# Optimization experiments

Measured on AMD Instinct MI355X. Metric: run time of the kernel, lower is better.

Reference implementation:

```python
import jax, jax.numpy as jnp
import numpy as np

DIM = 512
NUM_CLASSES = 2048
BATCH = 16384


def setup_inputs() -> dict:
    key = jax.random.key(0)
    kx, kc = jax.random.split(key)
    x = jax.random.normal(kx, (BATCH, DIM), dtype=jnp.float32)
    # torch.rand -> uniform [0,1)
    centers = jax.random.uniform(kc, (NUM_CLASSES, DIM), dtype=jnp.float32)
    return {"x": x, "centers": centers}


def reference(x, centers):
    x_sq = jnp.sum(x * x, axis=-1, keepdims=True)            # [B, 1]
    c_sq = jnp.sum(centers * centers, axis=-1)[None, :]      # [1, K]
    cross = jnp.einsum('bd,kd->bk', x, centers)              # [B, K]
    dist_sq = x_sq + c_sq - 2.0 * cross                      # [B, K]
    # responsibilities: stable softmax over -0.5 * dist_sq along classes
    resp = jax.nn.softmax(-0.5 * dist_sq, axis=-1)
    return resp
```

## Files before the change

### kernel.cpp

```cpp
#include <hip/hip_runtime.h>

#define BATCH 16384
#define DIM   512
#define NCLS  2048

typedef _Float16 half8 __attribute__((ext_vector_type(8)));
typedef float    floatx4 __attribute__((ext_vector_type(4)));

__global__ __launch_bounds__(256) void pack_b(const float* __restrict__ C,
                                              _Float16* __restrict__ BP) {
    int t = blockIdx.x * 256 + threadIdx.x;
    int lane = t & 63, ns = t >> 6;
    int s = ns & 15, n = ns >> 4;
    int col = n * 16 + (lane & 15);
    int k   = s * 32 + (lane >> 4) * 8;
    const float4* src = reinterpret_cast<const float4*>(C + (size_t)col * DIM + k);
    float4 a = src[0], b = src[1];
    half8 h;
    h[0] = (_Float16)a.x; h[1] = (_Float16)a.y; h[2] = (_Float16)a.z; h[3] = (_Float16)a.w;
    h[4] = (_Float16)b.x; h[5] = (_Float16)b.y; h[6] = (_Float16)b.z; h[7] = (_Float16)b.w;
    *reinterpret_cast<half8*>(BP + (size_t)t * 8) = h;
}

__global__ __launch_bounds__(64) void csq_kernel(const float* __restrict__ c,
                                                 float* __restrict__ hcsq) {
    int k = blockIdx.x, t = threadIdx.x;
    const float4* p = reinterpret_cast<const float4*>(c + (size_t)k * DIM);
    float s = 0.f;
    #pragma unroll
    for (int j = 0; j < 2; ++j) {
        float4 v = p[t + j * 64];
        s += v.x * v.x + v.y * v.y + v.z * v.z + v.w * v.w;
    }
    #pragma unroll
    for (int o = 32; o; o >>= 1) s += __shfl_xor(s, o);
    if (t == 0) hcsq[k] = 0.5f * s;
}

__global__ __launch_bounds__(512, 2) void fused_kernel(
    const float* __restrict__ X,
    const _Float16* __restrict__ BP,
    const float* __restrict__ hcsq,
    float* __restrict__ O)
{
    __shared__ __align__(16) _Float16 As[32 * 512];
    __shared__ float redm[8][32];
    __shared__ float rsum[8][32];

    const int tid  = threadIdx.x;
    const int lane = tid & 63;
    const int wave = tid >> 6;
    const int l4   = lane >> 4;
    const int r15  = lane & 15;

    for (int tile = 0; tile < 2; ++tile) {
        const int rowB = (blockIdx.x * 2 + tile) * 32;

        #pragma unroll
        for (int i = 0; i < 4; ++i) {
            int G = i * 512 + tid;
            int row = G >> 6, g = G & 63;
            const float* src = X + (size_t)(rowB + row) * DIM + g * 8;
            float4 a = *reinterpret_cast<const float4*>(src);
            float4 b = *reinterpret_cast<const float4*>(src + 4);
            half8 h;
            h[0] = (_Float16)a.x; h[1] = (_Float16)a.y; h[2] = (_Float16)a.z; h[3] = (_Float16)a.w;
            h[4] = (_Float16)b.x; h[5] = (_Float16)b.y; h[6] = (_Float16)b.z; h[7] = (_Float16)b.w;
            *reinterpret_cast<half8*>(&As[(row * 64 + (g ^ (row & 7))) * 8]) = h;
        }
        __syncthreads();

        floatx4 logv[4][2][4];
        float mj[2][4];
        #pragma unroll
        for (int rt = 0; rt < 2; ++rt)
            #pragma unroll
            for (int j = 0; j < 4; ++j) mj[rt][j] = -1e30f;

        #pragma unroll
        for (int chunk = 0; chunk < 4; ++chunk) {
            floatx4 acc[2][4];
            #pragma unroll
            for (int rt = 0; rt < 2; ++rt)
                #pragma unroll
                for (int ct = 0; ct < 4; ++ct)
                    acc[rt][ct] = (floatx4){0.f, 0.f, 0.f, 0.f};

            float hc[4];
            #pragma unroll
            for (int ct = 0; ct < 4; ++ct)
                hc[ct] = hcsq[chunk * 512 + wave * 64 + ct * 16 + r15];

            const _Float16* bb = BP + ((size_t)(chunk * 32 + wave * 4) * 1024 + lane) * 8;

            #pragma unroll 4
            for (int s = 0; s < 16; ++s) {
                half8 bf[4];
                #pragma unroll
                for (int ct = 0; ct < 4; ++ct)
                    bf[ct] = *reinterpret_cast<const half8*>(
                        bb + (size_t)((ct * 16 + s) * 64) * 8);
                const int kg = s * 4 + l4;
                const int sw = kg ^ (r15 & 7);
                half8 af0 = *reinterpret_cast<const half8*>(&As[(r15 * 64 + sw) * 8]);
                half8 af1 = *reinterpret_cast<const half8*>(&As[((16 + r15) * 64 + sw) * 8]);
                #pragma unroll
                for (int ct = 0; ct < 4; ++ct) {
                    acc[0][ct] = __builtin_amdgcn_mfma_f32_16x16x32_f16(af0, bf[ct], acc[0][ct], 0, 0, 0);
                    acc[1][ct] = __builtin_amdgcn_mfma_f32_16x16x32_f16(af1, bf[ct], acc[1][ct], 0, 0, 0);
                }
            }

            #pragma unroll
            for (int rt = 0; rt < 2; ++rt)
                #pragma unroll
                for (int ct = 0; ct < 4; ++ct) {
                    floatx4 v = acc[rt][ct];
                    #pragma unroll
                    for (int j = 0; j < 4; ++j) {
                        v[j] -= hc[ct];
                        mj[rt][j] = fmaxf(mj[rt][j], v[j]);
                    }
                    logv[chunk][rt][ct] = v;
                }
        }

        #pragma unroll
        for (int off = 8; off >= 1; off >>= 1)
            #pragma unroll
            for (int rt = 0; rt < 2; ++rt)
                #pragma unroll
                for (int j = 0; j < 4; ++j)
                    mj[rt][j] = fmaxf(mj[rt][j], __shfl_xor(mj[rt][j], off));
        if (r15 == 0) {
            #pragma unroll
            for (int rt = 0; rt < 2; ++rt)
                #pragma unroll
                for (int j = 0; j < 4; ++j)
                    redm[wave][rt * 16 + l4 * 4 + j] = mj[rt][j];
        }
        __syncthreads();

        float M[2][4];
        #pragma unroll
        for (int rt = 0; rt < 2; ++rt)
            #pragma unroll
            for (int j = 0; j < 4; ++j) {
                const int r = rt * 16 + l4 * 4 + j;
                float m = redm[0][r];
                #pragma unroll
                for (int w = 1; w < 8; ++w) m = fmaxf(m, redm[w][r]);
                M[rt][j] = m;
            }

        float tot[2][4];
        #pragma unroll
        for (int rt = 0; rt < 2; ++rt)
            #pragma unroll
            for (int j = 0; j < 4; ++j) tot[rt][j] = 0.f;
        #pragma unroll
        for (int chunk = 0; chunk < 4; ++chunk)
            #pragma unroll
            for (int rt = 0; rt < 2; ++rt)
                #pragma unroll
                for (int ct = 0; ct < 4; ++ct)
                    #pragma unroll
                    for (int j = 0; j < 4; ++j) {
                        float e = __expf(logv[chunk][rt][ct][j] - M[rt][j]);
                        logv[chunk][rt][ct][j] = e;
                        tot[rt][j] += e;
                    }
        #pragma unroll
        for (int off = 8; off >= 1; off >>= 1)
            #pragma unroll
            for (int rt = 0; rt < 2; ++rt)
                #pragma unroll
                for (int j = 0; j < 4; ++j)
                    tot[rt][j] += __shfl_xor(tot[rt][j], off);
        if (r15 == 0) {
            #pragma unroll
            for (int rt = 0; rt < 2; ++rt)
                #pragma unroll
                for (int j = 0; j < 4; ++j)
                    rsum[wave][rt * 16 + l4 * 4 + j] = tot[rt][j];
        }
        __syncthreads();

        float inv[2][4];
        #pragma unroll
        for (int rt = 0; rt < 2; ++rt)
            #pragma unroll
            for (int j = 0; j < 4; ++j) {
                const int r = rt * 16 + l4 * 4 + j;
                float ssum = 0.f;
                #pragma unroll
                for (int w = 0; w < 8; ++w) ssum += rsum[w][r];
                inv[rt][j] = 1.0f / ssum;
            }

        #pragma unroll
        for (int chunk = 0; chunk < 4; ++chunk)
            #pragma unroll
            for (int rt = 0; rt < 2; ++rt)
                #pragma unroll
                for (int ct = 0; ct < 4; ++ct) {
                    const int col = chunk * 512 + wave * 64 + ct * 16 + r15;
                    float* op = O + (size_t)(rowB + rt * 16 + l4 * 4) * NCLS + col;
                    #pragma unroll
                    for (int j = 0; j < 4; ++j)
                        op[(size_t)j * NCLS] = logv[chunk][rt][ct][j] * inv[rt][j];
                }
        __syncthreads();
    }
}

extern "C" void kernel_launch(void* const* d_in, const int* in_sizes, int n_in,
                              void* d_out, int out_size, void* d_ws, size_t ws_size,
                              hipStream_t stream) {
    const float* x       = (const float*)d_in[0];
    const float* centers = (const float*)d_in[1];
    float* out = (float*)d_out;

    _Float16* bp = (_Float16*)d_ws;
    float* hcsq  = (float*)(bp + (size_t)128 * 16 * 64 * 8);

    hipLaunchKernelGGL(pack_b, dim3(128 * 16 * 64 / 256), dim3(256), 0, stream, centers, bp);
    hipLaunchKernelGGL(csq_kernel, dim3(NCLS), dim3(64), 0, stream, centers, hcsq);
    hipLaunchKernelGGL(fused_kernel, dim3(BATCH / 64), dim3(512), 0, stream,
                       x, bp, hcsq, out);
}
```

Before: 110.9 us.

## Process 64-row tiles with online per-chunk softmax and bf16-packed exponentials

Each block now handles one 64-row tile with waves split 2 rows x 4 column groups, so each B fragment feeds twice as many rows. Exponentials are computed per chunk against a chunk-local max and kept as bf16 pairs, which halves register storage and lets all 2048 columns stay in registers. Chunk and k-step start offsets are staggered per block to spread L2 traffic. The cost is bf16 rounding of the stored probabilities and extra exp rescaling work in the epilogue.

Result: slower. 127.2 us (+14.7%).

```diff
diff --git a/kernel.cpp b/kernel.cpp
--- a/kernel.cpp
+++ b/kernel.cpp
@@ -6,6 +6,14 @@
 
 typedef _Float16 half8 __attribute__((ext_vector_type(8)));
 typedef float    floatx4 __attribute__((ext_vector_type(4)));
+
+__device__ inline unsigned pack2bf(float a, float b) {
+    unsigned ua = (__builtin_bit_cast(unsigned, a) + 0x8000u) >> 16;
+    unsigned ub = (__builtin_bit_cast(unsigned, b) + 0x8000u) >> 16;
+    return ua | (ub << 16);
+}
+__device__ inline float ubf_lo(unsigned u) { return __builtin_bit_cast(float, u << 16); }
+__device__ inline float ubf_hi(unsigned u) { return __builtin_bit_cast(float, u & 0xffff0000u); }
 
 __global__ __launch_bounds__(256) void pack_b(const float* __restrict__ C,
                                               _Float16* __restrict__ BP) {
@@ -43,174 +51,209 @@
     const float* __restrict__ hcsq,
     float* __restrict__ O)
 {
-    __shared__ __align__(16) _Float16 As[32 * 512];
-    __shared__ float redm[8][32];
-    __shared__ float rsum[8][32];
+    __shared__ __align__(16) _Float16 As[64 * 512];
+    __shared__ float redm[4][64];
+    __shared__ float rsum[4][64];
 
     const int tid  = threadIdx.x;
     const int lane = tid & 63;
     const int wave = tid >> 6;
+    const int rw   = wave & 1;
+    const int cg   = wave >> 1;
     const int l4   = lane >> 4;
     const int r15  = lane & 15;
-
-    for (int tile = 0; tile < 2; ++tile) {
-        const int rowB = (blockIdx.x * 2 + tile) * 32;
-
-        #pragma unroll
-        for (int i = 0; i < 4; ++i) {
-            int G = i * 512 + tid;
-            int row = G >> 6, g = G & 63;
-            const float* src = X + (size_t)(rowB + row) * DIM + g * 8;
-            float4 a = *reinterpret_cast<const float4*>(src);
-            float4 b = *reinterpret_cast<const float4*>(src + 4);
-            half8 h;
-            h[0] = (_Float16)a.x; h[1] = (_Float16)a.y; h[2] = (_Float16)a.z; h[3] = (_Float16)a.w;
-            h[4] = (_Float16)b.x; h[5] = (_Float16)b.y; h[6] = (_Float16)b.z; h[7] = (_Float16)b.w;
-            *reinterpret_cast<half8*>(&As[(row * 64 + (g ^ (row & 7))) * 8]) = h;
-        }
-        __syncthreads();
-
-        floatx4 logv[4][2][4];
-        float mj[2][4];
-        #pragma unroll
-        for (int rt = 0; rt < 2; ++rt)
-            #pragma unroll
-            for (int j = 0; j < 4; ++j) mj[rt][j] = -1e30f;
-
-        #pragma unroll
-        for (int chunk = 0; chunk < 4; ++chunk) {
-            floatx4 acc[2][4];
-            #pragma unroll
-            for (int rt = 0; rt < 2; ++rt)
+    const int rowB = blockIdx.x * 64;
+    const int stgc = (blockIdx.x >> 3) & 7;
+    const int stgs = (blockIdx.x >> 3) & 15;
+
+    #pragma unroll
+    for (int i = 0; i < 8; ++i) {
+        int G = i * 512 + tid;
+        int row = G >> 6, g = G & 63;
+        const float* src = X + (size_t)(rowB + row) * DIM + g * 8;
+        float4 a = *reinterpret_cast<const float4*>(src);
+        float4 b = *reinterpret_cast<const float4*>(src + 4);
+        half8 h;
+        h[0] = (_Float16)a.x; h[1] = (_Float16)a.y; h[2] = (_Float16)a.z; h[3] = (_Float16)a.w;
+        h[4] = (_Float16)b.x; h[5] = (_Float16)b.y; h[6] = (_Float16)b.z; h[7] = (_Float16)b.w;
+        *reinterpret_cast<half8*>(&As[(row * 64 + (g ^ (row & 7))) * 8]) = h;
+    }
+    __syncthreads();
+
+    unsigned ev[8][2][4][2];
+    unsigned mh[8][2][2];
+
+    #pragma unroll
+    for (int c0 = 0; c0 < 8; ++c0) {
+        const int ch = (c0 + stgc) & 7;
+
+        floatx4 acc[2][4];
+        #pragma unroll
+        for (int rt = 0; rt < 2; ++rt)
+            #pragma unroll
+            for (int ct = 0; ct < 4; ++ct)
+                acc[rt][ct] = (floatx4){0.f, 0.f, 0.f, 0.f};
+
+        float hc[4];
+        #pragma unroll
+        for (int ct = 0; ct < 4; ++ct)
+            hc[ct] = hcsq[ch * 256 + cg * 64 + ct * 16 + r15];
+
+        const _Float16* bb = BP + ((size_t)(ch * 16 + cg * 4) * 1024 + lane) * 8;
+
+        #pragma unroll 4
+        for (int s0 = 0; s0 < 16; ++s0) {
+            const int s = (s0 + stgs) & 15;
+            half8 bf[4];
+            #pragma unroll
+            for (int ct = 0; ct < 4; ++ct)
+                bf[ct] = *reinterpret_cast<const half8*>(
+                    bb + (size_t)((ct * 16 + s) * 64) * 8);
+            const int kg = s * 4 + l4;
+            const int sw = kg ^ (r15 & 7);
+            half8 af0 = *reinterpret_cast<const half8*>(
+                &As[((rw * 32 + r15) * 64 + sw) * 8]);
+            half8 af1 = *reinterpret_cast<const half8*>(
+                &As[((rw * 32 + 16 + r15) * 64 + sw) * 8]);
+            #pragma unroll
+            for (int ct = 0; ct < 4; ++ct) {
+                acc[0][ct] = __builtin_amdgcn_mfma_f32_16x16x32_f16(af0, bf[ct], acc[0][ct], 0, 0, 0);
+                acc[1][ct] = __builtin_amdgcn_mfma_f32_16x16x32_f16(af1, bf[ct], acc[1][ct], 0, 0, 0);
+            }
+        }
+
+        #pragma unroll
+        for (int rt = 0; rt < 2; ++rt) {
+            float l[4][4];
+            float mj[4] = {-1e30f, -1e30f, -1e30f, -1e30f};
+            #pragma unroll
+            for (int ct = 0; ct < 4; ++ct)
                 #pragma unroll
-                for (int ct = 0; ct < 4; ++ct)
-                    acc[rt][ct] = (floatx4){0.f, 0.f, 0.f, 0.f};
-
-            float hc[4];
-            #pragma unroll
-            for (int ct = 0; ct < 4; ++ct)
-                hc[ct] = hcsq[chunk * 512 + wave * 64 + ct * 16 + r15];
-
-            const _Float16* bb = BP + ((size_t)(chunk * 32 + wave * 4) * 1024 + lane) * 8;
-
-            #pragma unroll 4
-            for (int s = 0; s < 16; ++s) {
-                half8 bf[4];
-                #pragma unroll
-                for (int ct = 0; ct < 4; ++ct)
-                    bf[ct] = *reinterpret_cast<const half8*>(
-                        bb + (size_t)((ct * 16 + s) * 64) * 8);
-                const int kg = s * 4 + l4;
-                const int sw = kg ^ (r15 & 7);
-                half8 af0 = *reinterpret_cast<const half8*>(&As[(r15 * 64 + sw) * 8]);
-                half8 af1 = *reinterpret_cast<const half8*>(&As[((16 + r15) * 64 + sw) * 8]);
-                #pragma unroll
-                for (int ct = 0; ct < 4; ++ct) {
-                    acc[0][ct] = __builtin_amdgcn_mfma_f32_16x16x32_f16(af0, bf[ct], acc[0][ct], 0, 0, 0);
-                    acc[1][ct] = __builtin_amdgcn_mfma_f32_16x16x32_f16(af1, bf[ct], acc[1][ct], 0, 0, 0);
+                for (int j = 0; j < 4; ++j) {
+                    l[ct][j] = acc[rt][ct][j] - hc[ct];
+                    mj[j] = fmaxf(mj[j], l[ct][j]);
                 }
-            }
-
-            #pragma unroll
-            for (int rt = 0; rt < 2; ++rt)
-                #pragma unroll
-                for (int ct = 0; ct < 4; ++ct) {
-                    floatx4 v = acc[rt][ct];
-                    #pragma unroll
-                    for (int j = 0; j < 4; ++j) {
-                        v[j] -= hc[ct];
-                        mj[rt][j] = fmaxf(mj[rt][j], v[j]);
-                    }
-                    logv[chunk][rt][ct] = v;
-                }
-        }
-
-        #pragma unroll
-        for (int off = 8; off >= 1; off >>= 1)
-            #pragma unroll
-            for (int rt = 0; rt < 2; ++rt)
+            #pragma unroll
+            for (int off = 8; off >= 1; off >>= 1)
                 #pragma unroll
                 for (int j = 0; j < 4; ++j)
-                    mj[rt][j] = fmaxf(mj[rt][j], __shfl_xor(mj[rt][j], off));
-        if (r15 == 0) {
-            #pragma unroll
-            for (int rt = 0; rt < 2; ++rt)
-                #pragma unroll
-                for (int j = 0; j < 4; ++j)
-                    redm[wave][rt * 16 + l4 * 4 + j] = mj[rt][j];
-        }
-        __syncthreads();
-
-        float M[2][4];
-        #pragma unroll
-        for (int rt = 0; rt < 2; ++rt)
-            #pragma unroll
-            for (int j = 0; j < 4; ++j) {
-                const int r = rt * 16 + l4 * 4 + j;
-                float m = redm[0][r];
-                #pragma unroll
-                for (int w = 1; w < 8; ++w) m = fmaxf(m, redm[w][r]);
-                M[rt][j] = m;
-            }
-
-        float tot[2][4];
-        #pragma unroll
-        for (int rt = 0; rt < 2; ++rt)
-            #pragma unroll
-            for (int j = 0; j < 4; ++j) tot[rt][j] = 0.f;
-        #pragma unroll
-        for (int chunk = 0; chunk < 4; ++chunk)
-            #pragma unroll
-            for (int rt = 0; rt < 2; ++rt)
-                #pragma unroll
-                for (int ct = 0; ct < 4; ++ct)
-                    #pragma unroll
-                    for (int j = 0; j < 4; ++j) {
-                        float e = __expf(logv[chunk][rt][ct][j] - M[rt][j]);
-                        logv[chunk][rt][ct][j] = e;
-                        tot[rt][j] += e;
-                    }
-        #pragma unroll
-        for (int off = 8; off >= 1; off >>= 1)
-            #pragma unroll
-            for (int rt = 0; rt < 2; ++rt)
-                #pragma unroll
-                for (int j = 0; j < 4; ++j)
-                    tot[rt][j] += __shfl_xor(tot[rt][j], off);
-        if (r15 == 0) {
-            #pragma unroll
-            for (int rt = 0; rt < 2; ++rt)
-                #pragma unroll
-                for (int j = 0; j < 4; ++j)
-                    rsum[wave][rt * 16 + l4 * 4 + j] = tot[rt][j];
-        }
-        __syncthreads();
-
-        float inv[2][4];
-        #pragma unroll
-        for (int rt = 0; rt < 2; ++rt)
-            #pragma unroll
-            for (int j = 0; j < 4; ++j) {
-                const int r = rt * 16 + l4 * 4 + j;
-                float ssum = 0.f;
-                #pragma unroll
-                for (int w = 0; w < 8; ++w) ssum += rsum[w][r];
-                inv[rt][j] = 1.0f / ssum;
-            }
-
-        #pragma unroll
-        for (int chunk = 0; chunk < 4; ++chunk)
-            #pragma unroll
-            for (int rt = 0; rt < 2; ++rt)
-                #pragma unroll
-                for (int ct = 0; ct < 4; ++ct) {
-                    const int col = chunk * 512 + wave * 64 + ct * 16 + r15;
-                    float* op = O + (size_t)(rowB + rt * 16 + l4 * 4) * NCLS + col;
-                    #pragma unroll
-                    for (int j = 0; j < 4; ++j)
-                        op[(size_t)j * NCLS] = logv[chunk][rt][ct][j] * inv[rt][j];
-                }
-        __syncthreads();
+                    mj[j] = fmaxf(mj[j], __shfl_xor(mj[j], off));
+            unsigned m01 = pack2bf(mj[0], mj[1]);
+            unsigned m23 = pack2bf(mj[2], mj[3]);
+            mh[c0][rt][0] = m01;
+            mh[c0][rt][1] = m23;
+            float mb[4] = {ubf_lo(m01), ubf_hi(m01), ubf_lo(m23), ubf_hi(m23)};
+            #pragma unroll
+            for (int ct = 0; ct < 4; ++ct) {
+                float e0 = __expf(l[ct][0] - mb[0]);
+                float e1 = __expf(l[ct][1] - mb[1]);
+                float e2 = __expf(l[ct][2] - mb[2]);
+                float e3 = __expf(l[ct][3] - mb[3]);
+                ev[c0][rt][ct][0] = pack2bf(e0, e1);
+                ev[c0][rt][ct][1] = pack2bf(e2, e3);
+            }
+        }
+    }
+
+    float Ml[2][4];
+    #pragma unroll
+    for (int rt = 0; rt < 2; ++rt)
+        #pragma unroll
+        for (int j = 0; j < 4; ++j) Ml[rt][j] = -1e30f;
+    #pragma unroll
+    for (int c0 = 0; c0 < 8; ++c0)
+        #pragma unroll
+        for (int rt = 0; rt < 2; ++rt) {
+            Ml[rt][0] = fmaxf(Ml[rt][0], ubf_lo(mh[c0][rt][0]));
+            Ml[rt][1] = fmaxf(Ml[rt][1], ubf_hi(mh[c0][rt][0]));
+            Ml[rt][2] = fmaxf(Ml[rt][2], ubf_lo(mh[c0][rt][1]));
+            Ml[rt][3] = fmaxf(Ml[rt][3], ubf_hi(mh[c0][rt][1]));
+        }
+    if (r15 == 0) {
+        #pragma unroll
+        for (int rt = 0; rt < 2; ++rt)
+            #pragma unroll
+            for (int j = 0; j < 4; ++j)
+                redm[cg][rw * 32 + rt * 16 + l4 * 4 + j] = Ml[rt][j];
+    }
+    __syncthreads();
+
+    float M[2][4];
+    #pragma unroll
+    for (int rt = 0; rt < 2; ++rt)
+        #pragma unroll
+        for (int j = 0; j < 4; ++j) {
+            const int r = rw * 32 + rt * 16 + l4 * 4 + j;
+            M[rt][j] = fmaxf(fmaxf(redm[0][r], redm[1][r]),
+                             fmaxf(redm[2][r], redm[3][r]));
+        }
+
+    float tot[2][4] = {{0.f, 0.f, 0.f, 0.f}, {0.f, 0.f, 0.f, 0.f}};
+    #pragma unroll
+    for (int c0 = 0; c0 < 8; ++c0)
+        #pragma unroll
+        for (int rt = 0; rt < 2; ++rt) {
+            float sc[4];
+            sc[0] = __expf(ubf_lo(mh[c0][rt][0]) - M[rt][0]);
+            sc[1] = __expf(ubf_hi(mh[c0][rt][0]) - M[rt][1]);
+            sc[2] = __expf(ubf_lo(mh[c0][rt][1]) - M[rt][2]);
+            sc[3] = __expf(ubf_hi(mh[c0][rt][1]) - M[rt][3]);
+            float es[4] = {0.f, 0.f, 0.f, 0.f};
+            #pragma unroll
+            for (int ct = 0; ct < 4; ++ct) {
+                es[0] += ubf_lo(ev[c0][rt][ct][0]);
+                es[1] += ubf_hi(ev[c0][rt][ct][0]);
+                es[2] += ubf_lo(ev[c0][rt][ct][1]);
+                es[3] += ubf_hi(ev[c0][rt][ct][1]);
+            }
+            #pragma unroll
+            for (int j = 0; j < 4; ++j) tot[rt][j] += es[j] * sc[j];
+        }
+    #pragma unroll
+    for (int off = 8; off >= 1; off >>= 1)
+        #pragma unroll
+        for (int rt = 0; rt < 2; ++rt)
+            #pragma unroll
+            for (int j = 0; j < 4; ++j)
+                tot[rt][j] += __shfl_xor(tot[rt][j], off);
+    if (r15 == 0) {
+        #pragma unroll
+        for (int rt = 0; rt < 2; ++rt)
+            #pragma unroll
+            for (int j = 0; j < 4; ++j)
+                rsum[cg][rw * 32 + rt * 16 + l4 * 4 + j] = tot[rt][j];
+    }
+    __syncthreads();
+
+    float inv[2][4];
+    #pragma unroll
+    for (int rt = 0; rt < 2; ++rt)
+        #pragma unroll
+        for (int j = 0; j < 4; ++j) {
+            const int r = rw * 32 + rt * 16 + l4 * 4 + j;
+            inv[rt][j] = 1.0f / (rsum[0][r] + rsum[1][r] + rsum[2][r] + rsum[3][r]);
+        }
+
+    #pragma unroll
+    for (int c0 = 0; c0 < 8; ++c0) {
+        const int ch = (c0 + stgc) & 7;
+        #pragma unroll
+        for (int rt = 0; rt < 2; ++rt) {
+            float f[4];
+            f[0] = __expf(ubf_lo(mh[c0][rt][0]) - M[rt][0]) * inv[rt][0];
+            f[1] = __expf(ubf_hi(mh[c0][rt][0]) - M[rt][1]) * inv[rt][1];
+            f[2] = __expf(ubf_lo(mh[c0][rt][1]) - M[rt][2]) * inv[rt][2];
+            f[3] = __expf(ubf_hi(mh[c0][rt][1]) - M[rt][3]) * inv[rt][3];
+            #pragma unroll
+            for (int ct = 0; ct < 4; ++ct) {
+                const int col = ch * 256 + cg * 64 + ct * 16 + r15;
+                float* op = O + (size_t)(rowB + rw * 32 + rt * 16 + l4 * 4) * NCLS + col;
+                op[0 * (size_t)NCLS] = ubf_lo(ev[c0][rt][ct][0]) * f[0];
+                op[1 * (size_t)NCLS] = ubf_hi(ev[c0][rt][ct][0]) * f[1];
+                op[2 * (size_t)NCLS] = ubf_lo(ev[c0][rt][ct][1]) * f[2];
+                op[3 * (size_t)NCLS] = ubf_hi(ev[c0][rt][ct][1]) * f[3];
+            }
+        }
     }
 }
 
```
